# Kernel optimization log

Hardware: AMD Instinct MI355X
Metric: run time of the kernel (lower is better)

The kernel has to match this reference:

```python
import jax, jax.numpy as jnp
import numpy as np

V, S, L, H, D, DF = 32000, 2048, 8, 16, 1024, 4096
DH = D // H
EPS = jnp.finfo(jnp.float32).eps  # torch nn.RMSNorm(eps=None) uses finfo eps
STD = 0.02


def setup_inputs() -> dict:
    key = jax.random.key(0)
    ks = jax.random.split(key, 9)
    return {
        "input_ids": jax.random.randint(ks[0], (2, S), 0, V),
        "token_emb": jax.random.normal(ks[1], (V, D), dtype=jnp.float32) * STD,
        "pos_emb": jax.random.normal(ks[2], (S, D), dtype=jnp.float32) * STD,
        "wq": jax.random.normal(ks[3], (L, D, D), dtype=jnp.float32) * STD,
        "wk": jax.random.normal(ks[4], (L, D, D), dtype=jnp.float32) * STD,
        "wv": jax.random.normal(ks[5], (L, D, D), dtype=jnp.float32) * STD,
        "wo": jax.random.normal(ks[6], (L, D, D), dtype=jnp.float32) * STD,
        "w1": jax.random.normal(ks[7], (L, D, DF), dtype=jnp.float32) * STD,
        "w2": jax.random.normal(ks[8], (L, DF, D), dtype=jnp.float32) * STD,
        "attn_norm_w": jnp.ones((L, D), dtype=jnp.float32),
        "ffn_norm_w": jnp.ones((L, D), dtype=jnp.float32),
        "final_norm_w": jnp.ones((D,), dtype=jnp.float32),
    }


def _rmsnorm(x, w):
    return x * jax.lax.rsqrt(jnp.mean(x * x, axis=-1, keepdims=True) + EPS) * w


def reference(input_ids, token_emb, pos_emb, wq, wk, wv, wo, w1, w2,
              attn_norm_w, ffn_norm_w, final_norm_w):
    B, Sl = input_ids.shape
    x = token_emb[input_ids] + pos_emb[:Sl]                  # [B,S,D]
    mask = jnp.triu(jnp.full((Sl, Sl), -jnp.inf, dtype=x.dtype), k=1)
    scale = 1.0 / np.sqrt(DH)

    def block(x, p):
        Wq, Wk, Wv, Wo, W1, W2, anw, fnw = p
        h = _rmsnorm(x, anw)
        q = (h @ Wq).reshape(B, Sl, H, DH)
        k = (h @ Wk).reshape(B, Sl, H, DH)
        v = (h @ Wv).reshape(B, Sl, H, DH)
        scores = jnp.einsum('bqhd,bkhd->bhqk', q, k) * scale + mask
        probs = jax.nn.softmax(scores, axis=-1)
        attn = jnp.einsum('bhqk,bkhd->bqhd', probs, v).reshape(B, Sl, D)
        x = x + attn @ Wo
        h = _rmsnorm(x, fnw)
        x = x + jax.nn.gelu(h @ W1, approximate=False) @ W2  # F.gelu default = exact erf
        return x, None

    x, _ = jax.lax.scan(block, x, (wq, wk, wv, wo, w1, w2, attn_norm_w, ffn_norm_w))
    logits = _rmsnorm(x, final_norm_w) @ token_emb.T         # tied output projection
    return logits
```

## Files before the change

kernel.cpp:

```cpp
#include <hip/hip_runtime.h>
#include <math.h>

#define VOCAB 32000
#define SEQ 2048
#define NL 8
#define NH 16
#define DM 1024
#define DFF 4096
#define DH 64
#define NB 2
#define MM (NB*SEQ)

typedef __attribute__((ext_vector_type(4))) float f32x4;
typedef __attribute__((ext_vector_type(8))) short s16x8;

__device__ __forceinline__ ushort f2b(float f) {
  union { float f; unsigned u; } c; c.f = f;
  unsigned u = c.u;
  return (ushort)((u + 0x7fffu + ((u >> 16) & 1u)) >> 16);
}

__device__ __forceinline__ f32x4 mfma16(s16x8 a, s16x8 b, f32x4 c) {
  return __builtin_amdgcn_mfma_f32_16x16x32_bf16(a, b, c, 0, 0, 0);
}

__device__ __forceinline__ void gl_lds16(const ushort* g, ushort* l) {
  __builtin_amdgcn_global_load_lds((const __attribute__((address_space(1))) void*)g,
                                   (__attribute__((address_space(3))) void*)l, 16, 0, 0);
}

__global__ __launch_bounds__(256) void cast_kernel(const float* __restrict__ in,
                                                   ushort* __restrict__ out, int n4) {
  int i = blockIdx.x * 256 + threadIdx.x;
  if (i >= n4) return;
  float4 v = ((const float4*)in)[i];
  ushort4 o;
  o.x = f2b(v.x); o.y = f2b(v.y); o.z = f2b(v.z); o.w = f2b(v.w);
  ((ushort4*)out)[i] = o;
}

#define TP 68
__global__ __launch_bounds__(256) void tcast_kernel(const float* __restrict__ in,
                                                    ushort* __restrict__ out,
                                                    int Kd, int Nd) {
  __shared__ ushort t[64 * TP];
  const long base = (long)blockIdx.z * Kd * Nd;
  const int k0 = blockIdx.y * 64, n0 = blockIdx.x * 64;
  const int tid = threadIdx.x;
  #pragma unroll
  for (int i = 0; i < 4; i++) {
    int idx = i * 256 + tid;
    int r = idx >> 4, c = (idx & 15) << 2;
    float4 v = *(const float4*)(in + base + (long)(k0 + r) * Nd + n0 + c);
    t[r * TP + c + 0] = f2b(v.x);
    t[r * TP + c + 1] = f2b(v.y);
    t[r * TP + c + 2] = f2b(v.z);
    t[r * TP + c + 3] = f2b(v.w);
  }
  __syncthreads();
  #pragma unroll
  for (int i = 0; i < 4; i++) {
    int idx = i * 256 + tid;
    int rr = idx >> 4, c = (idx & 15) << 2;
    ushort4 o;
    o.x = t[(c + 0) * TP + rr];
    o.y = t[(c + 1) * TP + rr];
    o.z = t[(c + 2) * TP + rr];
    o.w = t[(c + 3) * TP + rr];
    *(ushort4*)(out + base + (long)(n0 + rr) * Kd + k0 + c) = o;
  }
}

__global__ __launch_bounds__(256) void embed_kernel(const int* __restrict__ ids,
                                                    const float* __restrict__ emb,
                                                    const float* __restrict__ pos,
                                                    float* __restrict__ x) {
  const int row = blockIdx.x;
  const int s = row & (SEQ - 1);
  const int id = ids[row];
  const float4* e = (const float4*)(emb + (long)id * DM);
  const float4* p = (const float4*)(pos + (long)s * DM);
  float4* o = (float4*)(x + (long)row * DM);
  int c = threadIdx.x;
  float4 a = e[c], b = p[c];
  float4 r; r.x = a.x + b.x; r.y = a.y + b.y; r.z = a.z + b.z; r.w = a.w + b.w;
  o[c] = r;
}

__global__ __launch_bounds__(256) void rmsnorm_kernel(const float* __restrict__ x,
                                                      const float* __restrict__ w,
                                                      ushort* __restrict__ out) {
  const int row = blockIdx.x;
  const int t = threadIdx.x;
  float4 v = ((const float4*)(x + (long)row * DM))[t];
  float ss = v.x*v.x + v.y*v.y + v.z*v.z + v.w*v.w;
  #pragma unroll
  for (int m = 1; m < 64; m <<= 1) ss += __shfl_xor(ss, m);
  __shared__ float sm[4];
  if ((t & 63) == 0) sm[t >> 6] = ss;
  __syncthreads();
  float tot = sm[0] + sm[1] + sm[2] + sm[3];
  float rr = rsqrtf(tot * (1.0f / DM) + 1.1920929e-07f);
  float4 wv = ((const float4*)w)[t];
  ushort4 o;
  o.x = f2b(v.x * rr * wv.x); o.y = f2b(v.y * rr * wv.y);
  o.z = f2b(v.z * rr * wv.z); o.w = f2b(v.w * rr * wv.w);
  ((ushort4*)out)[(long)row * (DM/4) + t] = o;
}

template<int MODE>
__global__ __launch_bounds__(256) void gemm_kernel(const ushort* __restrict__ A,
                                                   const ushort* __restrict__ Bm,
                                                   float* __restrict__ Cf,
                                                   ushort* __restrict__ Cb,
                                                   const float* __restrict__ R,
                                                   int Md, int Nd, int Kd) {
  __shared__ ushort sA[128 * 32];
  __shared__ ushort sB[128 * 32];
  const int tid = threadIdx.x;
  const int wave = tid >> 6, lane = tid & 63;
  const int quad = lane >> 4, l16 = lane & 15;
  const int wm = (wave >> 1) * 64, wn = (wave & 1) * 64;

  int bx = blockIdx.x, by = blockIdx.y;
  if (MODE == 0) {
    int nwg = gridDim.x * gridDim.y;
    int b = by * gridDim.x + bx;
    int q = nwg >> 3;
    int s = (b & 7) * q + (b >> 3);
    bx = s % gridDim.x; by = s / gridDim.x;
  }
  const long m0 = (long)by * 128, n0 = (long)bx * 128;

  const ushort* Ap = A + (m0 + wave * 32 + (lane >> 2)) * (long)Kd + ((lane & 3) << 3);
  const ushort* Bp = Bm + (n0 + wave * 32 + (lane >> 2)) * (long)Kd + ((lane & 3) << 3);
  ushort* sAw = sA + wave * 1024;
  ushort* sBw = sB + wave * 1024;
  const long rstep = 16 * (long)Kd;

  f32x4 acc[4][4];
  #pragma unroll
  for (int i = 0; i < 4; i++)
    #pragma unroll
    for (int j = 0; j < 4; j++) acc[i][j] = (f32x4){0.f, 0.f, 0.f, 0.f};

  for (long k0 = 0; k0 < Kd; k0 += 32) {
    __syncthreads();
    gl_lds16(Ap + k0, sAw);
    gl_lds16(Ap + k0 + rstep, sAw + 512);
    gl_lds16(Bp + k0, sBw);
    gl_lds16(Bp + k0 + rstep, sBw + 512);
    __syncthreads();
    s16x8 af[4], bf[4];
    #pragma unroll
    for (int mi = 0; mi < 4; mi++)
      af[mi] = *(const s16x8*)(sA + (wm + mi*16 + l16) * 32 + quad * 8);
    #pragma unroll
    for (int ni = 0; ni < 4; ni++)
      bf[ni] = *(const s16x8*)(sB + (wn + ni*16 + l16) * 32 + quad * 8);
    #pragma unroll
    for (int mi = 0; mi < 4; mi++)
      #pragma unroll
      for (int ni = 0; ni < 4; ni++)
        acc[mi][ni] = mfma16(af[mi], bf[ni], acc[mi][ni]);
  }

  #pragma unroll
  for (int mi = 0; mi < 4; mi++) {
    #pragma unroll
    for (int ni = 0; ni < 4; ni++) {
      #pragma unroll
      for (int r = 0; r < 4; r++) {
        long row = m0 + wm + mi*16 + quad*4 + r;
        long col = n0 + wn + ni*16 + l16;
        float v = acc[mi][ni][r];
        if (MODE == 0) {
          Cf[row * Nd + col] = v;
        } else if (MODE == 1) {
          Cf[row * Nd + col] = v + R[row * Nd + col];
        } else if (MODE == 2) {
          Cb[row * Nd + col] = f2b(v);
        } else {
          float g = 0.5f * v * (1.0f + erff(v * 0.70710678118654752f));
          Cb[row * Nd + col] = f2b(g);
        }
      }
    }
  }
}

__global__ __launch_bounds__(256) void attn_kernel(const ushort* __restrict__ Q,
                                                   const ushort* __restrict__ K,
                                                   const ushort* __restrict__ Vv,
                                                   ushort* __restrict__ O) {
  __shared__ ushort sP[4 * 16 * 32];
  const int wave = threadIdx.x >> 6, lane = threadIdx.x & 63;
  const int quad = lane >> 4, l16 = lane & 15;
  const int bh = blockIdx.y, b = bh >> 4, h = bh & 15;
  const int qb = blockIdx.x * 64 + wave * 16;
  const long rowbase = (long)b * SEQ;
  const int colbase = h * DH;

  const ushort* qp = Q + (rowbase + qb + l16) * (long)DM + colbase;
  s16x8 aq0 = *(const s16x8*)(qp + quad * 8);
  s16x8 aq1 = *(const s16x8*)(qp + 32 + quad * 8);

  f32x4 oacc[4];
  #pragma unroll
  for (int f = 0; f < 4; f++) oacc[f] = (f32x4){0.f, 0.f, 0.f, 0.f};
  float mr[4] = {-3.0e38f, -3.0e38f, -3.0e38f, -3.0e38f};
  float lr[4] = {0.f, 0.f, 0.f, 0.f};
  const f32x4 zero = (f32x4){0.f, 0.f, 0.f, 0.f};

  for (int kb = 0; kb <= qb + 15; kb += 32) {
    f32x4 sacc[2];
    #pragma unroll
    for (int c = 0; c < 2; c++) {
      const ushort* kp = K + (rowbase + kb + c*16 + l16) * (long)DM + colbase;
      s16x8 bk0 = *(const s16x8*)(kp + quad * 8);
      s16x8 bk1 = *(const s16x8*)(kp + 32 + quad * 8);
      sacc[c] = mfma16(aq0, bk0, zero);
      sacc[c] = mfma16(aq1, bk1, sacc[c]);
    }
    float p[2][4];
    #pragma unroll
    for (int r = 0; r < 4; r++) {
      int qrow = qb + quad*4 + r;
      #pragma unroll
      for (int c = 0; c < 2; c++) {
        int kcol = kb + c*16 + l16;
        float sv = sacc[c][r] * 0.125f;
        if (kcol > qrow) sv = -3.0e38f;
        p[c][r] = sv;
      }
      float t = fmaxf(p[0][r], p[1][r]);
      t = fmaxf(t, __shfl_xor(t, 1));
      t = fmaxf(t, __shfl_xor(t, 2));
      t = fmaxf(t, __shfl_xor(t, 4));
      t = fmaxf(t, __shfl_xor(t, 8));
      float newm = fmaxf(mr[r], t);
      float alpha = __expf(mr[r] - newm);
      mr[r] = newm;
      float pv0 = __expf(p[0][r] - newm);
      float pv1 = __expf(p[1][r] - newm);
      p[0][r] = pv0; p[1][r] = pv1;
      float rs = pv0 + pv1;
      rs += __shfl_xor(rs, 1);
      rs += __shfl_xor(rs, 2);
      rs += __shfl_xor(rs, 4);
      rs += __shfl_xor(rs, 8);
      lr[r] = lr[r] * alpha + rs;
      #pragma unroll
      for (int f = 0; f < 4; f++) oacc[f][r] *= alpha;
    }
    #pragma unroll
    for (int r = 0; r < 4; r++)
      #pragma unroll
      for (int c = 0; c < 2; c++)
        sP[wave * 512 + (quad*4 + r) * 32 + c*16 + l16] = f2b(p[c][r]);
    s16x8 ap = *(const s16x8*)(&sP[wave * 512 + l16 * 32 + quad * 8]);
    #pragma unroll
    for (int f = 0; f < 4; f++) {
      s16x8 bv;
      #pragma unroll
      for (int j = 0; j < 8; j++)
        bv[j] = (short)Vv[(rowbase + kb + quad*8 + j) * (long)DM + colbase + f*16 + l16];
      oacc[f] = mfma16(ap, bv, oacc[f]);
    }
  }
  #pragma unroll
  for (int f = 0; f < 4; f++) {
    #pragma unroll
    for (int r = 0; r < 4; r++) {
      long row = rowbase + qb + quad*4 + r;
      float inv = 1.0f / lr[r];
      O[row * (long)DM + colbase + f*16 + l16] = f2b(oacc[f][r] * inv);
    }
  }
}

extern "C" void kernel_launch(void* const* d_in, const int* in_sizes, int n_in,
                              void* d_out, int out_size, void* d_ws, size_t ws_size,
                              hipStream_t stream) {
  const int*   ids  = (const int*)d_in[0];
  const float* temb = (const float*)d_in[1];
  const float* pemb = (const float*)d_in[2];
  const float* wq   = (const float*)d_in[3];
  const float* wk   = (const float*)d_in[4];
  const float* wv   = (const float*)d_in[5];
  const float* wo   = (const float*)d_in[6];
  const float* w1   = (const float*)d_in[7];
  const float* w2   = (const float*)d_in[8];
  const float* anw  = (const float*)d_in[9];
  const float* fnw  = (const float*)d_in[10];
  const float* finw = (const float*)d_in[11];
  float* logits = (float*)d_out;

  char* p = (char*)d_ws;
  auto take = [&](size_t n) { char* r = p; p += (n + 255) & ~(size_t)255; return r; };
  ushort* wq_b = (ushort*)take((size_t)NL*DM*DM*2);
  ushort* wk_b = (ushort*)take((size_t)NL*DM*DM*2);
  ushort* wv_b = (ushort*)take((size_t)NL*DM*DM*2);
  ushort* wo_b = (ushort*)take((size_t)NL*DM*DM*2);
  ushort* w1_b = (ushort*)take((size_t)NL*DM*DFF*2);
  ushort* w2_b = (ushort*)take((size_t)NL*DFF*DM*2);
  ushort* te_b = (ushort*)take((size_t)VOCAB*DM*2);
  float*  x    = (float*) take((size_t)MM*DM*4);
  ushort* hb   = (ushort*)take((size_t)MM*DM*2);
  ushort* qbuf = (ushort*)take((size_t)MM*DM*2);
  ushort* kbuf = (ushort*)take((size_t)MM*DM*2);
  ushort* vbuf = (ushort*)take((size_t)MM*DM*2);
  ushort* abuf = (ushort*)take((size_t)MM*DM*2);
  ushort* gbuf = (ushort*)take((size_t)MM*DFF*2);

  tcast_kernel<<<dim3(DM/64,  DM/64,  NL), 256, 0, stream>>>(wq, wq_b, DM, DM);
  tcast_kernel<<<dim3(DM/64,  DM/64,  NL), 256, 0, stream>>>(wk, wk_b, DM, DM);
  tcast_kernel<<<dim3(DM/64,  DM/64,  NL), 256, 0, stream>>>(wv, wv_b, DM, DM);
  tcast_kernel<<<dim3(DM/64,  DM/64,  NL), 256, 0, stream>>>(wo, wo_b, DM, DM);
  tcast_kernel<<<dim3(DFF/64, DM/64,  NL), 256, 0, stream>>>(w1, w1_b, DM, DFF);
  tcast_kernel<<<dim3(DM/64,  DFF/64, NL), 256, 0, stream>>>(w2, w2_b, DFF, DM);
  {
    int n4 = (int)((size_t)VOCAB*DM / 4);
    cast_kernel<<<(n4 + 255) / 256, 256, 0, stream>>>(temb, te_b, n4);
  }

  embed_kernel<<<MM, 256, 0, stream>>>(ids, temb, pemb, x);

  dim3 gQ(DM/128, MM/128);
  dim3 gF(DFF/128, MM/128);
  for (int l = 0; l < NL; l++) {
    size_t o1 = (size_t)l * DM * DM, o2 = (size_t)l * DM * DFF;
    rmsnorm_kernel<<<MM, 256, 0, stream>>>(x, anw + (size_t)l*DM, hb);
    gemm_kernel<2><<<gQ, 256, 0, stream>>>(hb, wq_b + o1, nullptr, qbuf, nullptr, MM, DM, DM);
    gemm_kernel<2><<<gQ, 256, 0, stream>>>(hb, wk_b + o1, nullptr, kbuf, nullptr, MM, DM, DM);
    gemm_kernel<2><<<gQ, 256, 0, stream>>>(hb, wv_b + o1, nullptr, vbuf, nullptr, MM, DM, DM);
    attn_kernel<<<dim3(SEQ/64, NB*NH), 256, 0, stream>>>(qbuf, kbuf, vbuf, abuf);
    gemm_kernel<1><<<gQ, 256, 0, stream>>>(abuf, wo_b + o1, x, nullptr, x, MM, DM, DM);
    rmsnorm_kernel<<<MM, 256, 0, stream>>>(x, fnw + (size_t)l*DM, hb);
    gemm_kernel<3><<<gF, 256, 0, stream>>>(hb, w1_b + o2, nullptr, gbuf, nullptr, MM, DFF, DM);
    gemm_kernel<1><<<gQ, 256, 0, stream>>>(gbuf, w2_b + o2, x, nullptr, x, MM, DM, DFF);
  }
  rmsnorm_kernel<<<MM, 256, 0, stream>>>(x, finw, hb);
  gemm_kernel<0><<<dim3(VOCAB/128, MM/128), 256, 0, stream>>>(hb, te_b, logits, nullptr, nullptr, MM, VOCAB, DM);
}
```

Measured before the change: 5.406 ms.

## Fuse QKV GEMM, double-buffer GEMM LDS, transpose V, widen attention tiles

Q, K and V weights are packed into one matrix so a single GEMM produces Q and K into a shared buffer and writes V transposed. The attention kernel can then load V with vector reads instead of strided scalar gathers, and it now processes 64 keys per step with padded LDS. The GEMM main loop is double-buffered so global-to-LDS loads for the next k-step overlap the MFMAs, with one barrier per iteration instead of two. In exchange it uses twice the LDS, which may lower occupancy, and the transposed V store is strided.

```diff
diff --git a/kernel.cpp b/kernel.cpp
--- a/kernel.cpp
+++ b/kernel.cpp
@@ -42,16 +42,18 @@
 #define TP 68
 __global__ __launch_bounds__(256) void tcast_kernel(const float* __restrict__ in,
                                                     ushort* __restrict__ out,
-                                                    int Kd, int Nd) {
+                                                    int Kd, int Nd,
+                                                    long inLS, long outLS) {
   __shared__ ushort t[64 * TP];
-  const long base = (long)blockIdx.z * Kd * Nd;
+  const float* ip = in + (long)blockIdx.z * inLS;
+  ushort* op = out + (long)blockIdx.z * outLS;
   const int k0 = blockIdx.y * 64, n0 = blockIdx.x * 64;
   const int tid = threadIdx.x;
   #pragma unroll
   for (int i = 0; i < 4; i++) {
     int idx = i * 256 + tid;
     int r = idx >> 4, c = (idx & 15) << 2;
-    float4 v = *(const float4*)(in + base + (long)(k0 + r) * Nd + n0 + c);
+    float4 v = *(const float4*)(ip + (long)(k0 + r) * Nd + n0 + c);
     t[r * TP + c + 0] = f2b(v.x);
     t[r * TP + c + 1] = f2b(v.y);
     t[r * TP + c + 2] = f2b(v.z);
@@ -67,7 +69,7 @@
     o.y = t[(c + 1) * TP + rr];
     o.z = t[(c + 2) * TP + rr];
     o.w = t[(c + 3) * TP + rr];
-    *(ushort4*)(out + base + (long)(n0 + rr) * Kd + k0 + c) = o;
+    *(ushort4*)(op + (long)(n0 + rr) * Kd + k0 + c) = o;
   }
 }
 
@@ -113,10 +115,11 @@
                                                    const ushort* __restrict__ Bm,
                                                    float* __restrict__ Cf,
                                                    ushort* __restrict__ Cb,
+                                                   ushort* __restrict__ Ct,
                                                    const float* __restrict__ R,
                                                    int Md, int Nd, int Kd) {
-  __shared__ ushort sA[128 * 32];
-  __shared__ ushort sB[128 * 32];
+  __shared__ ushort sA[2][128 * 32];
+  __shared__ ushort sB[2][128 * 32];
   const int tid = threadIdx.x;
   const int wave = tid >> 6, lane = tid & 63;
   const int quad = lane >> 4, l16 = lane & 15;
@@ -134,35 +137,57 @@
 
   const ushort* Ap = A + (m0 + wave * 32 + (lane >> 2)) * (long)Kd + ((lane & 3) << 3);
   const ushort* Bp = Bm + (n0 + wave * 32 + (lane >> 2)) * (long)Kd + ((lane & 3) << 3);
-  ushort* sAw = sA + wave * 1024;
-  ushort* sBw = sB + wave * 1024;
+  const int ldso = wave * 1024;
   const long rstep = 16 * (long)Kd;
 
+  auto stage = [&](int buf, long k0) {
+    gl_lds16(Ap + k0, &sA[buf][ldso]);
+    gl_lds16(Ap + k0 + rstep, &sA[buf][ldso + 512]);
+    gl_lds16(Bp + k0, &sB[buf][ldso]);
+    gl_lds16(Bp + k0 + rstep, &sB[buf][ldso + 512]);
+  };
+
   f32x4 acc[4][4];
   #pragma unroll
   for (int i = 0; i < 4; i++)
     #pragma unroll
     for (int j = 0; j < 4; j++) acc[i][j] = (f32x4){0.f, 0.f, 0.f, 0.f};
 
+  stage(0, 0);
+  __syncthreads();
+  int cur = 0;
   for (long k0 = 0; k0 < Kd; k0 += 32) {
-    __syncthreads();
-    gl_lds16(Ap + k0, sAw);
-    gl_lds16(Ap + k0 + rstep, sAw + 512);
-    gl_lds16(Bp + k0, sBw);
-    gl_lds16(Bp + k0 + rstep, sBw + 512);
-    __syncthreads();
+    if (k0 + 32 < Kd) stage(cur ^ 1, k0 + 32);
     s16x8 af[4], bf[4];
     #pragma unroll
     for (int mi = 0; mi < 4; mi++)
-      af[mi] = *(const s16x8*)(sA + (wm + mi*16 + l16) * 32 + quad * 8);
+      af[mi] = *(const s16x8*)(&sA[cur][(wm + mi*16 + l16) * 32 + quad * 8]);
     #pragma unroll
     for (int ni = 0; ni < 4; ni++)
-      bf[ni] = *(const s16x8*)(sB + (wn + ni*16 + l16) * 32 + quad * 8);
+      bf[ni] = *(const s16x8*)(&sB[cur][(wn + ni*16 + l16) * 32 + quad * 8]);
     #pragma unroll
     for (int mi = 0; mi < 4; mi++)
       #pragma unroll
       for (int ni = 0; ni < 4; ni++)
         acc[mi][ni] = mfma16(af[mi], bf[ni], acc[mi][ni]);
+    __syncthreads();
+    cur ^= 1;
+  }
+
+  if (MODE == 5 && n0 >= 2048) {
+    #pragma unroll
+    for (int mi = 0; mi < 4; mi++) {
+      #pragma unroll
+      for (int ni = 0; ni < 4; ni++) {
+        long d = n0 + wn + ni*16 + l16 - 2048;
+        long row0 = m0 + wm + mi*16 + quad*4;
+        ushort4 o;
+        o.x = f2b(acc[mi][ni][0]); o.y = f2b(acc[mi][ni][1]);
+        o.z = f2b(acc[mi][ni][2]); o.w = f2b(acc[mi][ni][3]);
+        *(ushort4*)(Ct + d * MM + row0) = o;
+      }
+    }
+    return;
   }
 
   #pragma unroll
@@ -178,30 +203,31 @@
           Cf[row * Nd + col] = v;
         } else if (MODE == 1) {
           Cf[row * Nd + col] = v + R[row * Nd + col];
-        } else if (MODE == 2) {
-          Cb[row * Nd + col] = f2b(v);
-        } else {
+        } else if (MODE == 3) {
           float g = 0.5f * v * (1.0f + erff(v * 0.70710678118654752f));
           Cb[row * Nd + col] = f2b(g);
+        } else if (MODE == 5) {
+          Cb[row * 2048 + col] = f2b(v);
         }
       }
     }
   }
 }
 
-__global__ __launch_bounds__(256) void attn_kernel(const ushort* __restrict__ Q,
-                                                   const ushort* __restrict__ K,
-                                                   const ushort* __restrict__ Vv,
+#define SPLD 72
+__global__ __launch_bounds__(256) void attn_kernel(const ushort* __restrict__ QK,
+                                                   const ushort* __restrict__ Vt,
                                                    ushort* __restrict__ O) {
-  __shared__ ushort sP[4 * 16 * 32];
+  __shared__ ushort sP[4 * 16 * SPLD];
   const int wave = threadIdx.x >> 6, lane = threadIdx.x & 63;
   const int quad = lane >> 4, l16 = lane & 15;
   const int bh = blockIdx.y, b = bh >> 4, h = bh & 15;
   const int qb = blockIdx.x * 64 + wave * 16;
   const long rowbase = (long)b * SEQ;
   const int colbase = h * DH;
-
-  const ushort* qp = Q + (rowbase + qb + l16) * (long)DM + colbase;
+  ushort* sPw = sP + wave * 16 * SPLD;
+
+  const ushort* qp = QK + (rowbase + qb + l16) * 2048 + colbase;
   s16x8 aq0 = *(const s16x8*)(qp + quad * 8);
   s16x8 aq1 = *(const s16x8*)(qp + 32 + quad * 8);
 
@@ -212,28 +238,27 @@
   float lr[4] = {0.f, 0.f, 0.f, 0.f};
   const f32x4 zero = (f32x4){0.f, 0.f, 0.f, 0.f};
 
-  for (int kb = 0; kb <= qb + 15; kb += 32) {
-    f32x4 sacc[2];
-    #pragma unroll
-    for (int c = 0; c < 2; c++) {
-      const ushort* kp = K + (rowbase + kb + c*16 + l16) * (long)DM + colbase;
+  for (int kb = 0; kb <= qb + 15; kb += 64) {
+    f32x4 sacc[4];
+    #pragma unroll
+    for (int c = 0; c < 4; c++) {
+      const ushort* kp = QK + (rowbase + kb + c*16 + l16) * 2048 + 1024 + colbase;
       s16x8 bk0 = *(const s16x8*)(kp + quad * 8);
       s16x8 bk1 = *(const s16x8*)(kp + 32 + quad * 8);
       sacc[c] = mfma16(aq0, bk0, zero);
       sacc[c] = mfma16(aq1, bk1, sacc[c]);
     }
-    float p[2][4];
+    float p[4][4];
     #pragma unroll
     for (int r = 0; r < 4; r++) {
       int qrow = qb + quad*4 + r;
       #pragma unroll
-      for (int c = 0; c < 2; c++) {
+      for (int c = 0; c < 4; c++) {
         int kcol = kb + c*16 + l16;
         float sv = sacc[c][r] * 0.125f;
-        if (kcol > qrow) sv = -3.0e38f;
-        p[c][r] = sv;
+        p[c][r] = (kcol > qrow) ? -3.0e38f : sv;
       }
-      float t = fmaxf(p[0][r], p[1][r]);
+      float t = fmaxf(fmaxf(p[0][r], p[1][r]), fmaxf(p[2][r], p[3][r]));
       t = fmaxf(t, __shfl_xor(t, 1));
       t = fmaxf(t, __shfl_xor(t, 2));
       t = fmaxf(t, __shfl_xor(t, 4));
@@ -241,10 +266,9 @@
       float newm = fmaxf(mr[r], t);
       float alpha = __expf(mr[r] - newm);
       mr[r] = newm;
-      float pv0 = __expf(p[0][r] - newm);
-      float pv1 = __expf(p[1][r] - newm);
-      p[0][r] = pv0; p[1][r] = pv1;
-      float rs = pv0 + pv1;
+      float rs = 0.f;
+      #pragma unroll
+      for (int c = 0; c < 4; c++) { p[c][r] = __expf(p[c][r] - newm); rs += p[c][r]; }
       rs += __shfl_xor(rs, 1);
       rs += __shfl_xor(rs, 2);
       rs += __shfl_xor(rs, 4);
@@ -252,20 +276,19 @@
       lr[r] = lr[r] * alpha + rs;
       #pragma unroll
       for (int f = 0; f < 4; f++) oacc[f][r] *= alpha;
-    }
-    #pragma unroll
-    for (int r = 0; r < 4; r++)
-      #pragma unroll
-      for (int c = 0; c < 2; c++)
-        sP[wave * 512 + (quad*4 + r) * 32 + c*16 + l16] = f2b(p[c][r]);
-    s16x8 ap = *(const s16x8*)(&sP[wave * 512 + l16 * 32 + quad * 8]);
+      #pragma unroll
+      for (int c = 0; c < 4; c++)
+        sPw[(quad*4 + r) * SPLD + c*16 + l16] = f2b(p[c][r]);
+    }
+    s16x8 ap0 = *(const s16x8*)(&sPw[l16 * SPLD + quad * 8]);
+    s16x8 ap1 = *(const s16x8*)(&sPw[l16 * SPLD + 32 + quad * 8]);
     #pragma unroll
     for (int f = 0; f < 4; f++) {
-      s16x8 bv;
-      #pragma unroll
-      for (int j = 0; j < 8; j++)
-        bv[j] = (short)Vv[(rowbase + kb + quad*8 + j) * (long)DM + colbase + f*16 + l16];
-      oacc[f] = mfma16(ap, bv, oacc[f]);
+      const ushort* vp = Vt + (long)(colbase + f*16 + l16) * MM + rowbase + kb + quad*8;
+      s16x8 bv0 = *(const s16x8*)(vp);
+      s16x8 bv1 = *(const s16x8*)(vp + 32);
+      oacc[f] = mfma16(ap0, bv0, oacc[f]);
+      oacc[f] = mfma16(ap1, bv1, oacc[f]);
     }
   }
   #pragma unroll
@@ -298,27 +321,25 @@
 
   char* p = (char*)d_ws;
   auto take = [&](size_t n) { char* r = p; p += (n + 255) & ~(size_t)255; return r; };
-  ushort* wq_b = (ushort*)take((size_t)NL*DM*DM*2);
-  ushort* wk_b = (ushort*)take((size_t)NL*DM*DM*2);
-  ushort* wv_b = (ushort*)take((size_t)NL*DM*DM*2);
-  ushort* wo_b = (ushort*)take((size_t)NL*DM*DM*2);
-  ushort* w1_b = (ushort*)take((size_t)NL*DM*DFF*2);
-  ushort* w2_b = (ushort*)take((size_t)NL*DFF*DM*2);
-  ushort* te_b = (ushort*)take((size_t)VOCAB*DM*2);
-  float*  x    = (float*) take((size_t)MM*DM*4);
-  ushort* hb   = (ushort*)take((size_t)MM*DM*2);
-  ushort* qbuf = (ushort*)take((size_t)MM*DM*2);
-  ushort* kbuf = (ushort*)take((size_t)MM*DM*2);
-  ushort* vbuf = (ushort*)take((size_t)MM*DM*2);
-  ushort* abuf = (ushort*)take((size_t)MM*DM*2);
-  ushort* gbuf = (ushort*)take((size_t)MM*DFF*2);
-
-  tcast_kernel<<<dim3(DM/64,  DM/64,  NL), 256, 0, stream>>>(wq, wq_b, DM, DM);
-  tcast_kernel<<<dim3(DM/64,  DM/64,  NL), 256, 0, stream>>>(wk, wk_b, DM, DM);
-  tcast_kernel<<<dim3(DM/64,  DM/64,  NL), 256, 0, stream>>>(wv, wv_b, DM, DM);
-  tcast_kernel<<<dim3(DM/64,  DM/64,  NL), 256, 0, stream>>>(wo, wo_b, DM, DM);
-  tcast_kernel<<<dim3(DFF/64, DM/64,  NL), 256, 0, stream>>>(w1, w1_b, DM, DFF);
-  tcast_kernel<<<dim3(DM/64,  DFF/64, NL), 256, 0, stream>>>(w2, w2_b, DFF, DM);
+  ushort* wqkv_b = (ushort*)take((size_t)NL*3*DM*DM*2);
+  ushort* wo_b   = (ushort*)take((size_t)NL*DM*DM*2);
+  ushort* w1_b   = (ushort*)take((size_t)NL*DM*DFF*2);
+  ushort* w2_b   = (ushort*)take((size_t)NL*DFF*DM*2);
+  ushort* te_b   = (ushort*)take((size_t)VOCAB*DM*2);
+  float*  x      = (float*) take((size_t)MM*DM*4);
+  ushort* hb     = (ushort*)take((size_t)MM*DM*2);
+  ushort* qkbuf  = (ushort*)take((size_t)MM*2*DM*2);
+  ushort* vtbuf  = (ushort*)take((size_t)DM*MM*2);
+  ushort* abuf   = (ushort*)take((size_t)MM*DM*2);
+  ushort* gbuf   = (ushort*)take((size_t)MM*DFF*2);
+
+  const long LQ = (long)DM*DM, L3 = (long)3*DM*DM, LF = (long)DM*DFF;
+  tcast_kernel<<<dim3(DM/64,  DM/64,  NL), 256, 0, stream>>>(wq, wqkv_b,             DM, DM, LQ, L3);
+  tcast_kernel<<<dim3(DM/64,  DM/64,  NL), 256, 0, stream>>>(wk, wqkv_b + (long)DM*DM,   DM, DM, LQ, L3);
+  tcast_kernel<<<dim3(DM/64,  DM/64,  NL), 256, 0, stream>>>(wv, wqkv_b + (long)2*DM*DM, DM, DM, LQ, L3);
+  tcast_kernel<<<dim3(DM/64,  DM/64,  NL), 256, 0, stream>>>(wo, wo_b, DM, DM, LQ, LQ);
+  tcast_kernel<<<dim3(DFF/64, DM/64,  NL), 256, 0, stream>>>(w1, w1_b, DM, DFF, LF, LF);
+  tcast_kernel<<<dim3(DM/64,  DFF/64, NL), 256, 0, stream>>>(w2, w2_b, DFF, DM, LF, LF);
   {
     int n4 = (int)((size_t)VOCAB*DM / 4);
     cast_kernel<<<(n4 + 255) / 256, 256, 0, stream>>>(temb, te_b, n4);
@@ -326,20 +347,19 @@
 
   embed_kernel<<<MM, 256, 0, stream>>>(ids, temb, pemb, x);
 
+  dim3 gQKV(3*DM/128, MM/128);
   dim3 gQ(DM/128, MM/128);
   dim3 gF(DFF/128, MM/128);
   for (int l = 0; l < NL; l++) {
-    size_t o1 = (size_t)l * DM * DM, o2 = (size_t)l * DM * DFF;
+    size_t o3 = (size_t)l * 3*DM*DM, o1 = (size_t)l * DM * DM, o2 = (size_t)l * DM * DFF;
     rmsnorm_kernel<<<MM, 256, 0, stream>>>(x, anw + (size_t)l*DM, hb);
-    gemm_kernel<2><<<gQ, 256, 0, stream>>>(hb, wq_b + o1, nullptr, qbuf, nullptr, MM, DM, DM);
-    gemm_kernel<2><<<gQ, 256, 0, stream>>>(hb, wk_b + o1, nullptr, kbuf, nullptr, MM, DM, DM);
-    gemm_kernel<2><<<gQ, 256, 0, stream>>>(hb, wv_b + o1, nullptr, vbuf, nullptr, MM, DM, DM);
-    attn_kernel<<<dim3(SEQ/64, NB*NH), 256, 0, stream>>>(qbuf, kbuf, vbuf, abuf);
-    gemm_kernel<1><<<gQ, 256, 0, stream>>>(abuf, wo_b + o1, x, nullptr, x, MM, DM, DM);
+    gemm_kernel<5><<<gQKV, 256, 0, stream>>>(hb, wqkv_b + o3, nullptr, qkbuf, vtbuf, nullptr, MM, 3*DM, DM);
+    attn_kernel<<<dim3(SEQ/64, NB*NH), 256, 0, stream>>>(qkbuf, vtbuf, abuf);
+    gemm_kernel<1><<<gQ, 256, 0, stream>>>(abuf, wo_b + o1, x, nullptr, nullptr, x, MM, DM, DM);
     rmsnorm_kernel<<<MM, 256, 0, stream>>>(x, fnw + (size_t)l*DM, hb);
-    gemm_kernel<3><<<gF, 256, 0, stream>>>(hb, w1_b + o2, nullptr, gbuf, nullptr, MM, DFF, DM);
-    gemm_kernel<1><<<gQ, 256, 0, stream>>>(gbuf, w2_b + o2, x, nullptr, x, MM, DM, DFF);
+    gemm_kernel<3><<<gF, 256, 0, stream>>>(hb, w1_b + o2, nullptr, gbuf, nullptr, nullptr, MM, DFF, DM);
+    gemm_kernel<1><<<gQ, 256, 0, stream>>>(gbuf, w2_b + o2, x, nullptr, nullptr, x, MM, DM, DFF);
   }
   rmsnorm_kernel<<<MM, 256, 0, stream>>>(x, finw, hb);
-  gemm_kernel<0><<<dim3(VOCAB/128, MM/128), 256, 0, stream>>>(hb, te_b, logits, nullptr, nullptr, MM, VOCAB, DM);
-}
+  gemm_kernel<0><<<dim3(VOCAB/128, MM/128), 256, 0, stream>>>(hb, te_b, logits, nullptr, nullptr, nullptr, MM, VOCAB, DM);
+}
```

After: 5.032 ms. -6.9%, faster.
